# Optimization experiments

Hardware: AMD Instinct MI355X
Metric: run time of the kernel (lower is better)

Reference implementation:

```python
import jax, jax.numpy as jnp
import numpy as np

B, S, I, H, O = 256, 2048, 32, 128, 1


def setup_inputs() -> dict:
    key = jax.random.key(0)
    ks = jax.random.split(key, 9)
    sI = 1.0 / np.sqrt(I)
    sH = 1.0 / np.sqrt(H)
    sD = 1.0 / np.sqrt(H * S)
    return {
        "x": jax.random.normal(ks[0], (B, S, I), jnp.float32),
        "Wi": jax.random.normal(ks[1], (I, H), jnp.float32) * sI,
        "bi": jax.random.normal(ks[2], (H,), jnp.float32) * sI,
        "Wh": jax.random.normal(ks[3], (H, H), jnp.float32) * sH,
        "bh": jax.random.normal(ks[4], (H,), jnp.float32) * sH,
        "Wa": jax.random.normal(ks[5], (H, 1), jnp.float32) * sH,
        "ba": jax.random.normal(ks[6], (1,), jnp.float32) * sH,
        "Wd": jax.random.normal(ks[7], (H * S, O), jnp.float32) * sD,
        "bd": jax.random.normal(ks[8], (O,), jnp.float32) * sD,
        "resDepth": 4,
    }


def _branch_ids(seq_len: int, resDepth: int) -> np.ndarray:
    # Encodes the per-step branch of ResRNN_Cell.forward (static in i, resDepth):
    # 0: i==0 (set hstart, h0 stays zero)   1: i==lag-2 -> h0=tanh(hn+hstart)
    # 4: resDepth==1 -> h0=tanh(hn+h0)      2: i%resDepth==0 -> h0=tanh(hn+ht), ht=hn
    # 3: else -> h0=tanh(hn)
    br = np.full(seq_len, 3, dtype=np.int32)
    br[(np.arange(seq_len) % resDepth) == 0] = 2
    if resDepth == 1:
        br[:] = 4
    br[seq_len - 2] = 1
    br[0] = 0
    return br


def reference(x, Wi, bi, Wh, bh, Wa, ba, Wd, bd, resDepth):
    batch, seq_len, _ = x.shape
    hid = Wh.shape[0]
    br = _branch_ids(seq_len, int(resDepth))
    f0, f1, f2, f4 = (jnp.asarray(br == k) for k in (0, 1, 2, 4))
    xs = jnp.swapaxes(x, 0, 1)  # (S, B, I)
    z = jnp.zeros((batch, hid), x.dtype)

    def step(carry, inp):
        h0, ht, hstart = carry
        xt, g0, g1, g2, g4 = inp
        hn = xt @ Wi + bi + h0 @ Wh + bh  # (B, H)
        hstart = jnp.where(g0, hn, hstart)
        cand = jnp.where(g1, jnp.tanh(hn + hstart),
               jnp.where(g4, jnp.tanh(hn + h0),
               jnp.where(g2, jnp.tanh(hn + ht), jnp.tanh(hn))))
        h0n = jnp.where(g0, h0, cand)  # at i==0 h0 is NOT updated in the original
        htn = jnp.where(g2, hn, ht)
        return (h0n, htn, hstart), hn

    _, hiddens = jax.lax.scan(step, (z, z, z), (xs, f0, f1, f2, f4))
    # hiddens: (S, B, H) == torch.cat(outputs, 0)
    scores = hiddens @ Wa + ba  # (S, B, 1)
    # faithful to the original's .view((batchSize, -1)) on (S,B,1)-contiguous data
    att = jax.nn.softmax(scores.reshape(batch, seq_len), axis=-1)
    att = att.reshape(seq_len, batch, 1)
    weighted = hiddens * att  # (S, B, H)
    # faithful to .view(-1, hiddenNum * seq_len) on (S,B,H)-contiguous data
    flat = weighted.reshape(batch, seq_len * hid)
    return flat @ Wd + bd
```

## Files before the change

kernel.cpp:

```cpp
#include <hip/hip_runtime.h>
#include <math.h>

#define B_ 256
#define S_ 2048
#define I_ 32
#define H_ 128

__device__ __forceinline__ void sync_lds() {
    asm volatile("" ::: "memory");
    asm volatile("s_waitcnt lgkmcnt(0)" ::: "memory");
    __builtin_amdgcn_s_barrier();
    asm volatile("" ::: "memory");
}

__device__ __forceinline__ float fast_tanh(float z) {
    float e = __expf(2.0f * z);
    return 1.0f - 2.0f / (e + 1.0f);
}

template <int CTRL>
__device__ __forceinline__ float dppf(float v) {
    return __int_as_float(__builtin_amdgcn_update_dpp(
        0, __float_as_int(v), CTRL, 0xF, 0xF, false));
}

__device__ __forceinline__ float swz_xor16(float v) {
    return __int_as_float(__builtin_amdgcn_ds_swizzle(__float_as_int(v), 0x401F));
}

#define MAC1(hval, idx)                              \
    a0 = fmaf(hval, WhR[(idx) * 2 + 0], a0);         \
    a1 = fmaf(hval, WhR[(idx) * 2 + 1], a1);
#define MAC4(hv, j)                                  \
    MAC1((hv).x, 4 * (j) + 0)                        \
    MAC1((hv).y, 4 * (j) + 1)                        \
    MAC1((hv).z, 4 * (j) + 2)                        \
    MAC1((hv).w, 4 * (j) + 3)

#define UP_REDUCE(RING)                                                       \
    {                                                                         \
      float r = uP;                                                           \
      r += dppf<0xB1>(r);                                                     \
      r += dppf<0x124>(r);                                                    \
      if ((l & 0xD) == 0)                                                     \
        ((float*)&pl_lds[RING][(w << 2) | ((l >> 4) & 3)])[(l >> 1) & 1] = r; \
    }

#define PL_COMBINE(RING, SIDX)                                                \
    {                                                                         \
      float2 pp = pl_lds[RING][l & 31];                                       \
      float px = pp.x, py = pp.y;                                             \
      px += dppf<0xB1>(px);  py += dppf<0xB1>(py);                            \
      px += dppf<0x4E>(px);  py += dppf<0x4E>(py);                            \
      px += dppf<0x141>(px); py += dppf<0x141>(py);                           \
      px += dppf<0x128>(px); py += dppf<0x128>(py);                           \
      px += swz_xor16(px);   py += swz_xor16(py);                             \
      if (l == 0) part[((SIDX) << 8) + b] = make_float2(px, py);              \
    }

#define MAT_CORE(XA, XB)                                                      \
    float a0 = 0.f, a1 = 0.f;                                                 \
    MAC4(hv0, 0) MAC4(hv1, 1) MAC4(hv2, 2) MAC4(hv3, 3)                       \
    a0 += dppf<0xB1>(a0);                                                     \
    a1 += dppf<0xB1>(a1);                                                     \
    float tt = kb0b ? a1 : a0;                                                \
    float xwp = biasR;                                                        \
    xwp = fmaf((XA).x, WiC[0], xwp);                                          \
    xwp = fmaf((XA).y, WiC[1], xwp);                                          \
    xwp = fmaf((XA).z, WiC[2], xwp);                                          \
    xwp = fmaf((XA).w, WiC[3], xwp);                                          \
    xwp = fmaf((XB).x, WiC[4], xwp);                                          \
    xwp = fmaf((XB).y, WiC[5], xwp);                                          \
    xwp = fmaf((XB).z, WiC[6], xwp);                                          \
    xwp = fmaf((XB).w, WiC[7], xwp);                                          \
    tt += xwp;                                                                \
    tt += dppf<0x4E>(tt);                                                     \
    tt += dppf<0x128>(tt);                                                    \
    const float hn = tt;

#define STEP_FULL(g, PH, XA, XB, CPH)                                         \
  {                                                                           \
    const int s_ = (g) * 8 + (PH);                                            \
    const float4* hsrc = (const float4*)&h0_lds[(PH) & 1][0];                 \
    float4 hv0 = hsrc[kg];                                                    \
    float4 hv1 = hsrc[kg + 8];                                                \
    float4 hv2 = hsrc[kg + 16];                                               \
    float4 hv3 = hsrc[kg + 24];                                               \
    if (s_ >= 1) UP_REDUCE(((PH) + 3) & 3)                                    \
    if (w == (PH) && s_ >= 2) PL_COMBINE(((PH) + 2) & 3, s_ - 2)              \
    MAT_CORE(XA, XB)                                                          \
    if (s_ < S_ - 2) {                                                        \
      const float4* xr = (const float4*)(xgrp + ((PH) + 2) * I_);             \
      (XA) = xr[0]; (XB) = xr[1];                                             \
    }                                                                         \
    uP = hn * (CPH);                                                          \
    float h0n;                                                                \
    if (s_ == 0)            { hstartR = hn; h0n = 0.0f; }                     \
    else if (s_ == S_ - 2)  { h0n = fast_tanh(hn + hstartR); }                \
    else if (rd == 1)       { h0n = fast_tanh(hn + h0R); }                    \
    else if (cnt == 0)      { h0n = fast_tanh(hn + htR); htR = hn; }          \
    else                    { h0n = fast_tanh(hn); }                          \
    h0R = h0n;                                                                \
    if (wmask) h0_lds[((PH) + 1) & 1][hf] = h0n;                              \
    cnt = (cnt + 1 == rd) ? 0 : cnt + 1;                                      \
    sync_lds();                                                               \
  }

#define STEP_LEAN(g, PH, XA, XB, CPH)                                         \
  {                                                                           \
    const int s_ = (g) * 8 + (PH);                                            \
    const float4* hsrc = (const float4*)&h0_lds[(PH) & 1][0];                 \
    float4 hv0 = hsrc[kg];                                                    \
    float4 hv1 = hsrc[kg + 8];                                                \
    float4 hv2 = hsrc[kg + 16];                                               \
    float4 hv3 = hsrc[kg + 24];                                               \
    UP_REDUCE(((PH) + 3) & 3)                                                 \
    if (w == (PH)) PL_COMBINE(((PH) + 2) & 3, s_ - 2)                         \
    MAT_CORE(XA, XB)                                                          \
    {                                                                         \
      const float4* xr = (const float4*)(xgrp + ((PH) + 2) * I_);             \
      (XA) = xr[0]; (XB) = xr[1];                                             \
    }                                                                         \
    uP = hn * (CPH);                                                          \
    const bool c0 = (cnt == 0);                                               \
    float resid = rd1 ? h0R : (c0 ? htR : 0.0f);                              \
    float h0n = fast_tanh(hn + resid);                                        \
    htR = (htup && c0) ? hn : htR;                                            \
    h0R = h0n;                                                                \
    if (wmask) h0_lds[((PH) + 1) & 1][hf] = h0n;                              \
    cnt = (cnt + 1 == rd) ? 0 : cnt + 1;                                      \
    sync_lds();                                                               \
  }

__global__ __launch_bounds__(512)
__attribute__((amdgpu_waves_per_eu(2, 2)))
void rnn_kernel(
    const float* __restrict__ x, const float* __restrict__ Wi,
    const float* __restrict__ bi, const float* __restrict__ Wh,
    const float* __restrict__ bh, const float* __restrict__ Wa,
    const float* __restrict__ Wd, const int* __restrict__ rdp,
    float2* __restrict__ part)
{
    const int b = blockIdx.x;
    const int t = threadIdx.x;
    const int w = t >> 6;
    const int l = t & 63;
    const int  kg    = (l & 3) | (((l >> 3) & 1) << 2);
    const int  hg    = ((l >> 2) & 1) | (((l >> 4) & 1) << 1)
                     | (((l >> 5) & 1) << 2);
    const int  hbase = 16 * w + 2 * hg;
    const int  hf    = hbase + (l & 1);
    const bool kb0b  = (l & 1);
    const bool wmask = ((l & 0xA) == 0);
    const int  i0x   = 8 * (((l >> 1) & 1) | (((l >> 3) & 1) << 1));

    __shared__ __align__(16) float h0_lds[2][H_];
    __shared__ __align__(8)  float2 pl_lds[4][32];

    const int rd = rdp[0];
    const bool rd1  = (rd == 1);
    const bool htup = !rd1;
    if (t < H_) h0_lds[0][t] = 0.0f;

    float WhR[32];
#pragma unroll
    for (int j = 0; j < 4; ++j)
#pragma unroll
        for (int c = 0; c < 4; ++c) {
            int k = 4 * kg + 32 * j + c;
            float2 wv = *(const float2*)(Wh + (size_t)k * H_ + hbase);
            WhR[(4 * j + c) * 2 + 0] = wv.x;
            WhR[(4 * j + c) * 2 + 1] = wv.y;
        }
    float WiC[8];
#pragma unroll
    for (int i = 0; i < 8; ++i) WiC[i] = Wi[(size_t)(i0x + i) * H_ + hf];
    const float biasR = wmask ? (bi[hf] + bh[hf]) : 0.0f;

    const bool clsq = (l >> 1) & 1;
    const float waC = Wa[hf];
    float cph[8];
#pragma unroll
    for (int K = 0; K < 8; ++K)
        cph[K] = clsq ? Wd[(K << 15) + (b << 7) + hf] : waC;

    const float* xgrp = x + (size_t)b * (S_ * I_) + i0x;
    float4 xA0 = ((const float4*)xgrp)[0];
    float4 xB0 = ((const float4*)xgrp)[1];
    float4 xA1 = ((const float4*)(xgrp + I_))[0];
    float4 xB1 = ((const float4*)(xgrp + I_))[1];

    sync_lds();

    float htR = 0.f, hstartR = 0.f, h0R = 0.f;
    float uP = 0.f;
    int cnt = 0;

    {
        STEP_FULL(0, 0, xA0, xB0, cph[0])
        STEP_FULL(0, 1, xA1, xB1, cph[1])
        STEP_FULL(0, 2, xA0, xB0, cph[2])
        STEP_FULL(0, 3, xA1, xB1, cph[3])
        STEP_FULL(0, 4, xA0, xB0, cph[4])
        STEP_FULL(0, 5, xA1, xB1, cph[5])
        STEP_FULL(0, 6, xA0, xB0, cph[6])
        STEP_FULL(0, 7, xA1, xB1, cph[7])
        xgrp += 8 * I_;
    }
    for (int g = 1; g < 255; ++g) {
        STEP_LEAN(g, 0, xA0, xB0, cph[0])
        STEP_LEAN(g, 1, xA1, xB1, cph[1])
        STEP_LEAN(g, 2, xA0, xB0, cph[2])
        STEP_LEAN(g, 3, xA1, xB1, cph[3])
        STEP_LEAN(g, 4, xA0, xB0, cph[4])
        STEP_LEAN(g, 5, xA1, xB1, cph[5])
        STEP_LEAN(g, 6, xA0, xB0, cph[6])
        STEP_LEAN(g, 7, xA1, xB1, cph[7])
        xgrp += 8 * I_;
    }
    {
        STEP_FULL(255, 0, xA0, xB0, cph[0])
        STEP_FULL(255, 1, xA1, xB1, cph[1])
        STEP_FULL(255, 2, xA0, xB0, cph[2])
        STEP_FULL(255, 3, xA1, xB1, cph[3])
        STEP_FULL(255, 4, xA0, xB0, cph[4])
        STEP_FULL(255, 5, xA1, xB1, cph[5])
        STEP_FULL(255, 6, xA0, xB0, cph[6])
        STEP_FULL(255, 7, xA1, xB1, cph[7])
    }

    UP_REDUCE(3)
    sync_lds();
    if (w == 0) PL_COMBINE(2, S_ - 2)
    if (w == 1) PL_COMBINE(3, S_ - 1)
}

__global__ __launch_bounds__(256) void attn_kernel(
    const float2* __restrict__ part, const float* __restrict__ bd,
    float* __restrict__ out)
{
    const int r = blockIdx.x;
    const int t = threadIdx.x;
    float sc[8], dv[8];
    float mx = -1e30f;
#pragma unroll
    for (int u = 0; u < 8; ++u) {
        int f = (r << 11) + (u << 8) + t;
        float2 a = part[f];
        sc[u] = a.x;
        dv[u] = a.y;
        mx = fmaxf(mx, sc[u]);
    }
    __shared__ float redm[4], redz[4], redw[4];
#pragma unroll
    for (int off = 32; off > 0; off >>= 1) mx = fmaxf(mx, __shfl_xor(mx, off, 64));
    if ((t & 63) == 0) redm[t >> 6] = mx;
    __syncthreads();
    mx = fmaxf(fmaxf(redm[0], redm[1]), fmaxf(redm[2], redm[3]));
    float z = 0.f, wv = 0.f;
#pragma unroll
    for (int u = 0; u < 8; ++u) {
        float e = __expf(sc[u] - mx);
        z += e;
        wv += e * dv[u];
    }
#pragma unroll
    for (int off = 32; off > 0; off >>= 1) {
        z += __shfl_xor(z, off, 64);
        wv += __shfl_xor(wv, off, 64);
    }
    if ((t & 63) == 0) { redz[t >> 6] = z; redw[t >> 6] = wv; }
    __syncthreads();
    if (t == 0) {
        float Z = redz[0] + redz[1] + redz[2] + redz[3];
        float W = redw[0] + redw[1] + redw[2] + redw[3];
        out[r] = bd[0] + W / Z;
    }
}

extern "C" void kernel_launch(void* const* d_in, const int* in_sizes, int n_in,
                              void* d_out, int out_size, void* d_ws, size_t ws_size,
                              hipStream_t stream) {
    const float* x  = (const float*)d_in[0];
    const float* Wi = (const float*)d_in[1];
    const float* bi = (const float*)d_in[2];
    const float* Wh = (const float*)d_in[3];
    const float* bh = (const float*)d_in[4];
    const float* Wa = (const float*)d_in[5];
    const float* Wd = (const float*)d_in[7];
    const float* bd = (const float*)d_in[8];
    const int*  rdp = (const int*)d_in[9];

    float2* part = (float2*)d_ws;

    rnn_kernel<<<B_, 512, 0, stream>>>(x, Wi, bi, Wh, bh, Wa, Wd, rdp, part);
    attn_kernel<<<B_, 256, 0, stream>>>(part, bd, (float*)d_out);
}
```

Before: 929.4 us.

## Use packed FP32 FMAs for the recurrence matvec and specialize the resDepth-4 loop

Replaces the scalar FMA chains for the Wh matvec and the Wi input projection with v_pk_fma_f32 inline asm on paired weight registers, halving the FMA instruction count on the serial per-step critical path. Adds a dedicated main loop for resDepth==4 where the residual branch is resolved at compile time from the step phase, which drops the runtime counter and select logic. This adds code size and an extra partial-sum add. Also the h0R register is no longer updated inside that loop, which is safe only because h0R is read solely when resDepth is 1.

```diff
diff --git a/kernel.cpp b/kernel.cpp
--- a/kernel.cpp
+++ b/kernel.cpp
@@ -5,6 +5,21 @@
 #define S_ 2048
 #define I_ 32
 #define H_ 128
+
+typedef float v2f __attribute__((ext_vector_type(2)));
+__device__ __forceinline__ v2f mk2(float a, float b) { v2f r; r.x = a; r.y = b; return r; }
+
+__device__ __forceinline__ void pk_fma(v2f& d, v2f a, v2f b) {
+    asm("v_pk_fma_f32 %0, %1, %2, %0" : "+v"(d) : "v"(a), "v"(b));
+}
+__device__ __forceinline__ void pk_fma_lo(v2f& d, v2f a, v2f b) {
+    asm("v_pk_fma_f32 %0, %1, %2, %0 op_sel:[0,0,0] op_sel_hi:[0,1,1]"
+        : "+v"(d) : "v"(a), "v"(b));
+}
+__device__ __forceinline__ void pk_fma_hi(v2f& d, v2f a, v2f b) {
+    asm("v_pk_fma_f32 %0, %1, %2, %0 op_sel:[1,0,0] op_sel_hi:[1,1,1]"
+        : "+v"(d) : "v"(a), "v"(b));
+}
 
 __device__ __forceinline__ void sync_lds() {
     asm volatile("" ::: "memory");
@@ -28,14 +43,11 @@
     return __int_as_float(__builtin_amdgcn_ds_swizzle(__float_as_int(v), 0x401F));
 }
 
-#define MAC1(hval, idx)                              \
-    a0 = fmaf(hval, WhR[(idx) * 2 + 0], a0);         \
-    a1 = fmaf(hval, WhR[(idx) * 2 + 1], a1);
-#define MAC4(hv, j)                                  \
-    MAC1((hv).x, 4 * (j) + 0)                        \
-    MAC1((hv).y, 4 * (j) + 1)                        \
-    MAC1((hv).z, 4 * (j) + 2)                        \
-    MAC1((hv).w, 4 * (j) + 3)
+#define PKQ(hv, q)                                                \
+    pk_fma_lo(accA, mk2((hv).x, (hv).y), WhP[4 * (q) + 0]);       \
+    pk_fma_hi(accA, mk2((hv).x, (hv).y), WhP[4 * (q) + 1]);       \
+    pk_fma_lo(accB, mk2((hv).z, (hv).w), WhP[4 * (q) + 2]);       \
+    pk_fma_hi(accB, mk2((hv).z, (hv).w), WhP[4 * (q) + 3]);
 
 #define UP_REDUCE(RING)                                                       \
     {                                                                         \
@@ -59,21 +71,19 @@
     }
 
 #define MAT_CORE(XA, XB)                                                      \
-    float a0 = 0.f, a1 = 0.f;                                                 \
-    MAC4(hv0, 0) MAC4(hv1, 1) MAC4(hv2, 2) MAC4(hv3, 3)                       \
+    v2f xw01 = mk2(biasR, 0.0f);                                              \
+    pk_fma(xw01, mk2((XA).x, (XA).y), WiP[0]);                                \
+    pk_fma(xw01, mk2((XA).z, (XA).w), WiP[1]);                                \
+    pk_fma(xw01, mk2((XB).x, (XB).y), WiP[2]);                                \
+    pk_fma(xw01, mk2((XB).z, (XB).w), WiP[3]);                                \
+    v2f accA = mk2(0.0f, 0.0f), accB = mk2(0.0f, 0.0f);                       \
+    PKQ(hv0, 0) PKQ(hv1, 1) PKQ(hv2, 2) PKQ(hv3, 3)                           \
+    float a0 = accA.x + accB.x;                                               \
+    float a1 = accA.y + accB.y;                                               \
     a0 += dppf<0xB1>(a0);                                                     \
     a1 += dppf<0xB1>(a1);                                                     \
     float tt = kb0b ? a1 : a0;                                                \
-    float xwp = biasR;                                                        \
-    xwp = fmaf((XA).x, WiC[0], xwp);                                          \
-    xwp = fmaf((XA).y, WiC[1], xwp);                                          \
-    xwp = fmaf((XA).z, WiC[2], xwp);                                          \
-    xwp = fmaf((XA).w, WiC[3], xwp);                                          \
-    xwp = fmaf((XB).x, WiC[4], xwp);                                          \
-    xwp = fmaf((XB).y, WiC[5], xwp);                                          \
-    xwp = fmaf((XB).z, WiC[6], xwp);                                          \
-    xwp = fmaf((XB).w, WiC[7], xwp);                                          \
-    tt += xwp;                                                                \
+    tt += xw01.x + xw01.y;                                                    \
     tt += dppf<0x4E>(tt);                                                     \
     tt += dppf<0x128>(tt);                                                    \
     const float hn = tt;
@@ -106,16 +116,37 @@
     sync_lds();                                                               \
   }
 
-#define STEP_LEAN(g, PH, XA, XB, CPH)                                         \
+#define STEP_LEAN4(g, PH, XA, XB, CPH)                                        \
   {                                                                           \
-    const int s_ = (g) * 8 + (PH);                                            \
     const float4* hsrc = (const float4*)&h0_lds[(PH) & 1][0];                 \
     float4 hv0 = hsrc[kg];                                                    \
     float4 hv1 = hsrc[kg + 8];                                                \
     float4 hv2 = hsrc[kg + 16];                                               \
     float4 hv3 = hsrc[kg + 24];                                               \
     UP_REDUCE(((PH) + 3) & 3)                                                 \
-    if (w == (PH)) PL_COMBINE(((PH) + 2) & 3, s_ - 2)                         \
+    if (w == (PH)) PL_COMBINE(((PH) + 2) & 3, (g) * 8 + (PH) - 2)             \
+    MAT_CORE(XA, XB)                                                          \
+    {                                                                         \
+      const float4* xr = (const float4*)(xgrp + ((PH) + 2) * I_);             \
+      (XA) = xr[0]; (XB) = xr[1];                                             \
+    }                                                                         \
+    uP = hn * (CPH);                                                          \
+    float h0n;                                                                \
+    if (((PH) & 3) == 0) { h0n = fast_tanh(hn + htR); htR = hn; }             \
+    else                 { h0n = fast_tanh(hn); }                             \
+    if (wmask) h0_lds[((PH) + 1) & 1][hf] = h0n;                              \
+    sync_lds();                                                               \
+  }
+
+#define STEP_LEAN(g, PH, XA, XB, CPH)                                         \
+  {                                                                           \
+    const float4* hsrc = (const float4*)&h0_lds[(PH) & 1][0];                 \
+    float4 hv0 = hsrc[kg];                                                    \
+    float4 hv1 = hsrc[kg + 8];                                                \
+    float4 hv2 = hsrc[kg + 16];                                               \
+    float4 hv3 = hsrc[kg + 24];                                               \
+    UP_REDUCE(((PH) + 3) & 3)                                                 \
+    if (w == (PH)) PL_COMBINE(((PH) + 2) & 3, (g) * 8 + (PH) - 2)             \
     MAT_CORE(XA, XB)                                                          \
     {                                                                         \
       const float4* xr = (const float4*)(xgrp + ((PH) + 2) * I_);             \
@@ -162,19 +193,22 @@
     const bool htup = !rd1;
     if (t < H_) h0_lds[0][t] = 0.0f;
 
-    float WhR[32];
+    v2f WhP[16];
 #pragma unroll
     for (int j = 0; j < 4; ++j)
 #pragma unroll
         for (int c = 0; c < 4; ++c) {
             int k = 4 * kg + 32 * j + c;
             float2 wv = *(const float2*)(Wh + (size_t)k * H_ + hbase);
-            WhR[(4 * j + c) * 2 + 0] = wv.x;
-            WhR[(4 * j + c) * 2 + 1] = wv.y;
+            WhP[4 * j + c] = mk2(wv.x, wv.y);
         }
-    float WiC[8];
-#pragma unroll
-    for (int i = 0; i < 8; ++i) WiC[i] = Wi[(size_t)(i0x + i) * H_ + hf];
+    v2f WiP[4];
+#pragma unroll
+    for (int j = 0; j < 4; ++j) {
+        float w0 = Wi[(size_t)(i0x + 2 * j) * H_ + hf];
+        float w1 = Wi[(size_t)(i0x + 2 * j + 1) * H_ + hf];
+        WiP[j] = mk2(w0, w1);
+    }
     const float biasR = wmask ? (bi[hf] + bh[hf]) : 0.0f;
 
     const bool clsq = (l >> 1) & 1;
@@ -207,16 +241,31 @@
         STEP_FULL(0, 7, xA1, xB1, cph[7])
         xgrp += 8 * I_;
     }
-    for (int g = 1; g < 255; ++g) {
-        STEP_LEAN(g, 0, xA0, xB0, cph[0])
-        STEP_LEAN(g, 1, xA1, xB1, cph[1])
-        STEP_LEAN(g, 2, xA0, xB0, cph[2])
-        STEP_LEAN(g, 3, xA1, xB1, cph[3])
-        STEP_LEAN(g, 4, xA0, xB0, cph[4])
-        STEP_LEAN(g, 5, xA1, xB1, cph[5])
-        STEP_LEAN(g, 6, xA0, xB0, cph[6])
-        STEP_LEAN(g, 7, xA1, xB1, cph[7])
-        xgrp += 8 * I_;
+    if (rd == 4) {
+        for (int g = 1; g < 255; ++g) {
+            STEP_LEAN4(g, 0, xA0, xB0, cph[0])
+            STEP_LEAN4(g, 1, xA1, xB1, cph[1])
+            STEP_LEAN4(g, 2, xA0, xB0, cph[2])
+            STEP_LEAN4(g, 3, xA1, xB1, cph[3])
+            STEP_LEAN4(g, 4, xA0, xB0, cph[4])
+            STEP_LEAN4(g, 5, xA1, xB1, cph[5])
+            STEP_LEAN4(g, 6, xA0, xB0, cph[6])
+            STEP_LEAN4(g, 7, xA1, xB1, cph[7])
+            xgrp += 8 * I_;
+        }
+        cnt = 0;
+    } else {
+        for (int g = 1; g < 255; ++g) {
+            STEP_LEAN(g, 0, xA0, xB0, cph[0])
+            STEP_LEAN(g, 1, xA1, xB1, cph[1])
+            STEP_LEAN(g, 2, xA0, xB0, cph[2])
+            STEP_LEAN(g, 3, xA1, xB1, cph[3])
+            STEP_LEAN(g, 4, xA0, xB0, cph[4])
+            STEP_LEAN(g, 5, xA1, xB1, cph[5])
+            STEP_LEAN(g, 6, xA0, xB0, cph[6])
+            STEP_LEAN(g, 7, xA1, xB1, cph[7])
+            xgrp += 8 * I_;
+        }
     }
     {
         STEP_FULL(255, 0, xA0, xB0, cph[0])
```

After: 863.4 us. -7.1%, faster.
